# Kernel tuning notes

Measured on AMD Instinct MI355X. Metric: run time of the kernel, lower is better.

## Reference

```python
import jax, jax.numpy as jnp
import numpy as np

B, LQ, LK, H = 8, 2048, 2048, 1024


def setup_inputs() -> dict:
    key = jax.random.key(0)
    kq, kk, kv, km, kw = jax.random.split(key, 5)
    input_Q = jax.random.normal(kq, (B, LQ, H), dtype=jnp.float32)
    input_K = jax.random.normal(kk, (B, LK, H), dtype=jnp.float32)
    input_V = jax.random.normal(kv, (B, LK, H), dtype=jnp.float32)
    mask = jax.random.randint(km, (B, LK), 0, 2, dtype=jnp.int32)
    # learned parameter w_omega [H, H]; scaled init so scores are O(1)-ish
    w_omega = jax.random.normal(kw, (H, H), dtype=jnp.float32) * (H ** -0.5)
    return {"input_Q": input_Q, "input_K": input_K, "input_V": input_V,
            "w_omega": w_omega, "mask": mask}


def reference(input_Q, input_K, input_V, w_omega, mask):
    # att_input = Q @ W : [B, Lq, H]
    att_input = jnp.einsum('bqh,hd->bqd', input_Q, w_omega)
    # scores = att_input @ K^T : [B, Lq, Lk]
    att_scores = jnp.einsum('bqd,bkd->bqk', att_input, input_K)
    # masked fill with -inf where mask == 0 (mask broadcast over query dim)
    neg_inf = jnp.asarray(-jnp.inf, dtype=att_scores.dtype)
    scores = jnp.where(mask[:, None, :] == 0, neg_inf, att_scores)
    probs_softmax = jax.nn.softmax(scores, axis=-1)          # [B, Lq, Lk]
    probs_sigmoid = jax.nn.sigmoid(scores)                   # sigmoid(-inf)=0
    probs_sigmoid_hat = (probs_sigmoid > 0.5).astype(probs_softmax.dtype)
    att_output_softmax = jnp.einsum('bqk,bkh->bqh', probs_softmax, input_V)
    att_output_sigmoid = jnp.einsum('bqk,bkh->bqh', probs_sigmoid_hat, input_V)
    # torch .squeeze(1) is a no-op here since Lq > 1
    return (att_output_softmax, att_output_sigmoid, probs_softmax, probs_sigmoid)
```

## Files before the change

kernel.cpp:

```cpp
#include <hip/hip_runtime.h>
#include <math.h>

#define B_  8
#define LQ_ 2048
#define LK_ 2048
#define H_  1024

#define TAU      4e-3f
#define FIX_CAP  32768
#define FIX_E    8
#define SCL      256.0f
#define SCLQ     16.0f
#define INV_SS   (1.0f / 1048576.0f)

#define KBLK 512

typedef unsigned short ushort_t;
typedef __attribute__((ext_vector_type(8))) _Float16 v8h;
typedef __attribute__((ext_vector_type(8))) short  v8s;
typedef __attribute__((ext_vector_type(4))) float  v4f;
typedef __attribute__((ext_vector_type(4))) float  f4;
typedef __attribute__((ext_vector_type(4))) int    i4;
typedef __attribute__((ext_vector_type(4))) short  s4;

#if defined(__has_builtin)
#if __has_builtin(__builtin_amdgcn_global_load_lds)
#define HAS_GLDS 1
#endif
#endif

__device__ __forceinline__ ushort_t f2bf(float x) {
  unsigned u = __float_as_uint(x);
  u = (u + 0x7FFFu + ((u >> 16) & 1u)) >> 16;
  return (ushort_t)u;
}
__device__ __forceinline__ void split2h(float x, ushort_t& h, ushort_t& l) {
  union { _Float16 f; ushort_t u; } a, b;
  a.f = (_Float16)x;
  b.f = (_Float16)(x - (float)a.f);
  h = a.u; l = b.u;
}

__device__ __forceinline__ void gld_lds16(void* lds_dst, const void* g_src) {
#ifdef HAS_GLDS
  __builtin_amdgcn_global_load_lds((const __attribute__((address_space(1))) void*)g_src,
                                   (__attribute__((address_space(3))) void*)lds_dst,
                                   16, 0, 0);
#else
  *(i4*)lds_dst = *(const i4*)g_src;
#endif
}

__global__ void k_zero(int* p) { *p = 0; }

__global__ void k_split(const float* __restrict__ x, ushort_t* __restrict__ hi,
                        ushort_t* __restrict__ lo, int n4, float scale) {
  int stride = gridDim.x * blockDim.x;
  for (int i = blockIdx.x * blockDim.x + threadIdx.x; i < n4; i += stride) {
    f4 v = ((const f4*)x)[i];
    s4 h, l;
#pragma unroll
    for (int j = 0; j < 4; j++) {
      ushort_t hb, lb; split2h(v[j] * scale, hb, lb);
      h[j] = (short)hb; l[j] = (short)lb;
    }
    ((s4*)hi)[i] = h;
    ((s4*)lo)[i] = l;
  }
}

template <int SPLIT>
__global__ void k_transpose(const float* __restrict__ X, ushort_t* __restrict__ Yhi,
                            ushort_t* __restrict__ Ylo, int R, int C, float scale) {
  __shared__ float t[32][33];
  const int b = blockIdx.z;
  const float* Xb = X + (size_t)b * R * C;
  ushort_t* Yh = Yhi + (size_t)b * R * C;
  const int c0 = blockIdx.x * 32, r0 = blockIdx.y * 32;
  const int tx = threadIdx.x, ty = threadIdx.y;
#pragma unroll
  for (int i = 0; i < 4; i++)
    t[ty + 8 * i][tx] = Xb[(size_t)(r0 + ty + 8 * i) * C + c0 + tx];
  __syncthreads();
#pragma unroll
  for (int i = 0; i < 4; i++) {
    float v = t[tx][ty + 8 * i] * scale;
    size_t o = (size_t)(c0 + ty + 8 * i) * R + r0 + tx;
    if (SPLIT) {
      ushort_t h, l; split2h(v, h, l);
      Yh[o] = h;
      (Ylo + (size_t)b * R * C)[o] = l;
    } else {
      Yh[o] = f2bf(v);
    }
  }
}


template <int EPI>
__global__ __launch_bounds__(256, 2)
void gemm_hx2(const ushort_t* __restrict__ Ahi, const ushort_t* __restrict__ Alo,
              const ushort_t* __restrict__ Bhi, const ushort_t* __restrict__ Blo,
              int KD, long strideAB, long strideBB, int N,
              ushort_t* __restrict__ OutHi, ushort_t* __restrict__ OutLo, long strideOB,
              float* __restrict__ S, float* __restrict__ G, ushort_t* __restrict__ Hatb,
              const int* __restrict__ mask, int* __restrict__ cnt, int* __restrict__ flist) {
  const int b  = blockIdx.z;
  const int m0 = blockIdx.y * 128;
  const int n0 = blockIdx.x * 128;
  const ushort_t* Ah = Ahi + (size_t)b * strideAB + (size_t)m0 * KD;
  const ushort_t* Al = Alo + (size_t)b * strideAB + (size_t)m0 * KD;
  const ushort_t* Bh = Bhi + (size_t)b * strideBB + (size_t)n0 * KD;
  const ushort_t* Bl = Blo + (size_t)b * strideBB + (size_t)n0 * KD;

  __shared__ ushort_t sAh[128 * 32], sAl[128 * 32], sBh[128 * 32], sBl[128 * 32];

  const int tid  = threadIdx.x;
  const int lane = tid & 63;
  const int wid  = tid >> 6;
  const int wm   = (wid >> 1) * 64;
  const int wn   = (wid & 1) * 64;

  v4f acc[4][4] = {};

  const int r1 = tid >> 2;
  const int c1 = (tid & 3) ^ ((tid >> 3) & 3);
  const size_t go1 = (size_t)r1 * KD + (size_t)(c1 * 8);
  const size_t go2 = (size_t)(r1 + 64) * KD + (size_t)(c1 * 8);
  const int ldst1 = tid * 16;
  const int ldst2 = 4096 + tid * 16;

  const int fr = lane & 15;
  const int cq = lane >> 4;

  for (int k0 = 0; k0 < KD; k0 += 32) {
    __syncthreads();
    gld_lds16((char*)sAh + ldst1, Ah + go1 + k0);
    gld_lds16((char*)sAh + ldst2, Ah + go2 + k0);
    gld_lds16((char*)sAl + ldst1, Al + go1 + k0);
    gld_lds16((char*)sAl + ldst2, Al + go2 + k0);
    gld_lds16((char*)sBh + ldst1, Bh + go1 + k0);
    gld_lds16((char*)sBh + ldst2, Bh + go2 + k0);
    gld_lds16((char*)sBl + ldst1, Bl + go1 + k0);
    gld_lds16((char*)sBl + ldst2, Bl + go2 + k0);
    __syncthreads();

    v8h a_h[4], a_l[4], b_h[4], b_l[4];
#pragma unroll
    for (int i = 0; i < 4; i++) {
      const int Ra = wm + i * 16 + fr;
      const int ca = Ra * 32 + (((cq ^ ((Ra >> 1) & 3))) << 3);
      a_h[i] = *(const v8h*)&sAh[ca];
      a_l[i] = *(const v8h*)&sAl[ca];
      const int Rb = wn + i * 16 + fr;
      const int cb = Rb * 32 + (((cq ^ ((Rb >> 1) & 3))) << 3);
      b_h[i] = *(const v8h*)&sBh[cb];
      b_l[i] = *(const v8h*)&sBl[cb];
    }
#pragma unroll
    for (int i = 0; i < 4; i++)
#pragma unroll
      for (int j = 0; j < 4; j++) {
        acc[i][j] = __builtin_amdgcn_mfma_f32_16x16x32_f16(a_h[i], b_h[j], acc[i][j], 0, 0, 0);
        acc[i][j] = __builtin_amdgcn_mfma_f32_16x16x32_f16(a_h[i], b_l[j], acc[i][j], 0, 0, 0);
        acc[i][j] = __builtin_amdgcn_mfma_f32_16x16x32_f16(a_l[i], b_h[j], acc[i][j], 0, 0, 0);
      }
  }

  const int rg = (lane >> 4) * 4;
#pragma unroll
  for (int i = 0; i < 4; i++)
#pragma unroll
    for (int j = 0; j < 4; j++)
#pragma unroll
      for (int r = 0; r < 4; r++) {
        const int grow = m0 + wm + i * 16 + rg + r;
        const int gcol = n0 + wn + j * 16 + fr;
        const float v = acc[i][j][r];
        if (EPI == 0) {
          size_t o = (size_t)b * strideOB + (size_t)grow * N + gcol;
          ushort_t h, l; split2h(v, h, l);
          OutHi[o] = h; OutLo[o] = l;
        } else {
          size_t o = ((size_t)b * LQ_ + grow) * N + gcol;
          const float sv = v * INV_SS;
          S[o] = sv;
          int mk = mask[b * N + gcol];
          const float g = mk ? 1.0f / (1.0f + expf(-sv)) : 0.0f;
          G[o] = g;
          Hatb[o] = (g > 0.5f) ? (ushort_t)0x3F80 : (ushort_t)0;
          if (mk && fabsf(sv) < TAU) {
            int idx = atomicAdd(cnt, 1);
            if (idx < FIX_CAP) flist[idx] = (b << 22) | (grow << 11) | gcol;
          }
        }
      }
}

__global__ __launch_bounds__(256)
void k_fix_blas(const int* __restrict__ cnt, const int* __restrict__ flist,
                const float* __restrict__ Q, const float* __restrict__ Kx,
                const float* __restrict__ W, float* __restrict__ S,
                float* __restrict__ G, ushort_t* __restrict__ Hatb) {
  const int n = min(*cnt, FIX_CAP);
  const int base = blockIdx.x * FIX_E;
  if (base >= n) return;
  const int ne = min(FIX_E, n - base);
  const int tid = threadIdx.x;

  __shared__ float qs[FIX_E][H_];
  __shared__ float aA[FIX_E][H_];
  __shared__ int   ent[FIX_E];

  if (tid < FIX_E) ent[tid] = flist[base + ((tid < ne) ? tid : 0)];
  __syncthreads();

  for (int e = 0; e < FIX_E; e++) {
    const int en = ent[e];
    const int b = en >> 22, q = (en >> 11) & 2047;
    const float* Qr = Q + ((size_t)b * LQ_ + q) * H_;
    for (int i = tid; i < H_; i += 256) qs[e][i] = Qr[i];
  }
  __syncthreads();

  float atot[FIX_E][4];
  float acc[FIX_E][4];
  const float* Wp = W + tid * 4;
#pragma unroll
  for (int blk = 0; blk < 2; blk++) {
    const int h0 = blk * KBLK;
    const int h1 = h0 + KBLK;
#pragma unroll
    for (int e = 0; e < FIX_E; e++)
#pragma unroll
      for (int j = 0; j < 4; j++) acc[e][j] = 0.f;
    for (int h = h0; h < h1; h++) {
      f4 w = *(const f4*)(Wp + (size_t)h * H_);
#pragma unroll
      for (int e = 0; e < FIX_E; e++) {
        const float qv = qs[e][h];
        acc[e][0] = fmaf(qv, w[0], acc[e][0]);
        acc[e][1] = fmaf(qv, w[1], acc[e][1]);
        acc[e][2] = fmaf(qv, w[2], acc[e][2]);
        acc[e][3] = fmaf(qv, w[3], acc[e][3]);
      }
    }
#pragma unroll
    for (int e = 0; e < FIX_E; e++)
#pragma unroll
      for (int j = 0; j < 4; j++)
        atot[e][j] = (blk == 0) ? acc[e][j] : __fadd_rn(atot[e][j], acc[e][j]);
  }
#pragma unroll
  for (int e = 0; e < FIX_E; e++) {
    aA[e][tid * 4 + 0] = atot[e][0];
    aA[e][tid * 4 + 1] = atot[e][1];
    aA[e][tid * 4 + 2] = atot[e][2];
    aA[e][tid * 4 + 3] = atot[e][3];
  }
  __syncthreads();

  if (tid < ne) {
    const int e = tid;
    const int en = ent[e];
    const int b = en >> 22, q = (en >> 11) & 2047, k = en & 2047;
    const float* Kr = Kx + ((size_t)b * LK_ + k) * H_;
    const float* Ar = aA[e];
    float stot = 0.f;
#pragma unroll
    for (int blk = 0; blk < 2; blk++) {
      const int d0 = blk * KBLK;
      const int d1 = d0 + KBLK;
      float a = 0.f;
#pragma unroll 16
      for (int d = d0; d < d1; d++) a = fmaf(Ar[d], Kr[d], a);
      stot = (blk == 0) ? a : __fadd_rn(stot, a);
    }
    size_t o = ((size_t)b * LQ_ + q) * LK_ + k;
    S[o] = stot;
    const float g = 1.0f / (1.0f + expf(-stot));
    G[o] = g;
    Hatb[o] = (g > 0.5f) ? (ushort_t)0x3F80 : (ushort_t)0;
  }
}

__global__ void k_softmax(float* __restrict__ S, const int* __restrict__ mask,
                          ushort_t* __restrict__ Pb) {
  const int row = blockIdx.x;
  const int b   = row >> 11;
  float* Sr = S + (size_t)row * LK_;
  const int* mr = mask + b * LK_;
  const int tid = threadIdx.x;
  const int c0 = tid * 8;

  float v[8]; int mk[8];
  f4 v0 = *(const f4*)&Sr[c0];
  f4 v1 = *(const f4*)&Sr[c0 + 4];
  i4 m0 = *(const i4*)&mr[c0];
  i4 m1 = *(const i4*)&mr[c0 + 4];
#pragma unroll
  for (int j = 0; j < 4; j++) { v[j] = v0[j]; v[4 + j] = v1[j]; mk[j] = m0[j]; mk[4 + j] = m1[j]; }

  float mx = -INFINITY;
#pragma unroll
  for (int j = 0; j < 8; j++) if (mk[j]) mx = fmaxf(mx, v[j]);
#pragma unroll
  for (int off = 32; off; off >>= 1) mx = fmaxf(mx, __shfl_xor(mx, off));
  __shared__ float redm[4], reds[4];
  const int lane = tid & 63, wid = tid >> 6;
  if (lane == 0) redm[wid] = mx;
  __syncthreads();
  mx = fmaxf(fmaxf(redm[0], redm[1]), fmaxf(redm[2], redm[3]));

  float e[8], sum = 0.f;
#pragma unroll
  for (int j = 0; j < 8; j++) { e[j] = mk[j] ? expf(v[j] - mx) : 0.f; sum += e[j]; }
#pragma unroll
  for (int off = 32; off; off >>= 1) sum += __shfl_xor(sum, off);
  if (lane == 0) reds[wid] = sum;
  __syncthreads();
  sum = reds[0] + reds[1] + reds[2] + reds[3];
  const float inv = 1.0f / sum;

  f4 o0, o1;
  v8s pb;
#pragma unroll
  for (int j = 0; j < 4; j++) {
    o0[j] = e[j] * inv; o1[j] = e[4 + j] * inv;
    pb[j] = (short)f2bf(o0[j]); pb[4 + j] = (short)f2bf(o1[j]);
  }
  *(f4*)&Sr[c0] = o0;
  *(f4*)&Sr[c0 + 4] = o1;
  *(v8s*)&Pb[(size_t)row * LK_ + c0] = pb;
}

__global__ __launch_bounds__(256, 2)
void gemm_pvb(const ushort_t* __restrict__ A, const ushort_t* __restrict__ Bt,
              float* __restrict__ O) {
  const int b  = blockIdx.z;
  const int m0 = blockIdx.y * 128;
  const int n0 = blockIdx.x * 128;
  const ushort_t* Ab = A  + ((size_t)b * LQ_ + m0) * (size_t)LK_;
  const ushort_t* Bb = Bt + ((size_t)b * H_  + n0) * (size_t)LK_;

  __shared__ ushort_t sA[128 * 32], sB[128 * 32];

  const int tid  = threadIdx.x;
  const int lane = tid & 63;
  const int wid  = tid >> 6;
  const int wm   = (wid >> 1) * 64;
  const int wn   = (wid & 1) * 64;

  v4f acc[4][4] = {};

  const int r1 = tid >> 2;
  const int c1 = (tid & 3) ^ ((tid >> 3) & 3);
  const size_t go1 = (size_t)r1 * LK_ + (size_t)(c1 * 8);
  const size_t go2 = (size_t)(r1 + 64) * LK_ + (size_t)(c1 * 8);
  const int ldst1 = tid * 16;
  const int ldst2 = 4096 + tid * 16;

  const int fr = lane & 15;
  const int cq = lane >> 4;

  for (int k0 = 0; k0 < LK_; k0 += 32) {
    __syncthreads();
    gld_lds16((char*)sA + ldst1, Ab + go1 + k0);
    gld_lds16((char*)sA + ldst2, Ab + go2 + k0);
    gld_lds16((char*)sB + ldst1, Bb + go1 + k0);
    gld_lds16((char*)sB + ldst2, Bb + go2 + k0);
    __syncthreads();

    v8s af[4], bf[4];
#pragma unroll
    for (int i = 0; i < 4; i++) {
      const int Ra = wm + i * 16 + fr;
      af[i] = *(const v8s*)&sA[Ra * 32 + ((cq ^ ((Ra >> 1) & 3)) << 3)];
      const int Rb = wn + i * 16 + fr;
      bf[i] = *(const v8s*)&sB[Rb * 32 + ((cq ^ ((Rb >> 1) & 3)) << 3)];
    }
#pragma unroll
    for (int i = 0; i < 4; i++)
#pragma unroll
      for (int j = 0; j < 4; j++)
        acc[i][j] = __builtin_amdgcn_mfma_f32_16x16x32_bf16(af[i], bf[j], acc[i][j], 0, 0, 0);
  }

  const int rg = (lane >> 4) * 4;
#pragma unroll
  for (int i = 0; i < 4; i++)
#pragma unroll
    for (int j = 0; j < 4; j++)
#pragma unroll
      for (int r = 0; r < 4; r++) {
        const int grow = m0 + wm + i * 16 + rg + r;
        const int gcol = n0 + wn + j * 16 + fr;
        O[((size_t)b * LQ_ + grow) * H_ + gcol] = acc[i][j][r];
      }
}

extern "C" void kernel_launch(void* const* d_in, const int* in_sizes, int n_in,
                              void* d_out, int out_size, void* d_ws, size_t ws_size,
                              hipStream_t stream) {
  const float* Q = (const float*)d_in[0];
  const float* K = (const float*)d_in[1];
  const float* V = (const float*)d_in[2];
  const float* W = (const float*)d_in[3];
  const int* mask = (const int*)d_in[4];

  float* out0 = (float*)d_out;
  float* out1 = out0 + (size_t)B_ * LQ_ * H_;
  float* out2 = out1 + (size_t)B_ * LQ_ * H_;
  float* out3 = out2 + (size_t)B_ * LQ_ * LK_;

  const size_t NQ = (size_t)B_ * LQ_ * H_;
  char* ws = (char*)d_ws;
  int* cnt   = (int*)ws;                    ws += 256;
  int* flist = (int*)ws;                    ws += FIX_CAP * 4;
  ushort_t* Qhi = (ushort_t*)ws;            ws += NQ * 2;
  ushort_t* Qlo = (ushort_t*)ws;            ws += NQ * 2;
  ushort_t* Khi = (ushort_t*)ws;            ws += NQ * 2;
  ushort_t* Klo = (ushort_t*)ws;            ws += NQ * 2;
  ushort_t* Ahi = (ushort_t*)ws;            ws += NQ * 2;
  ushort_t* Alo = (ushort_t*)ws;            ws += NQ * 2;
  ushort_t* Vt  = (ushort_t*)ws;            ws += NQ * 2;
  ushort_t* Wthi = (ushort_t*)ws;           ws += (size_t)H_ * H_ * 2;
  ushort_t* Wtlo = (ushort_t*)ws;

  ushort_t* hatb = Qhi;
  ushort_t* Pb   = Ahi;

  k_zero<<<1, 1, 0, stream>>>(cnt);

  k_split<<<2048, 256, 0, stream>>>(Q, Qhi, Qlo, (int)(NQ / 4), SCLQ);
  k_split<<<2048, 256, 0, stream>>>(K, Khi, Klo, (int)(NQ / 4), SCL);
  dim3 tb(32, 8);
  k_transpose<1><<<dim3(32, 32, 1), tb, 0, stream>>>(W, Wthi, Wtlo, H_, H_, SCL);
  k_transpose<0><<<dim3(32, 64, B_), tb, 0, stream>>>(V, Vt, nullptr, LK_, H_, 1.0f);

  gemm_hx2<0><<<dim3(H_ / 128, LQ_ / 128, B_), 256, 0, stream>>>(
      Qhi, Qlo, Wthi, Wtlo, H_, (long)LQ_ * H_, 0L, H_,
      Ahi, Alo, (long)LQ_ * H_, nullptr, nullptr, nullptr, nullptr, nullptr, nullptr);

  gemm_hx2<1><<<dim3(LK_ / 128, LQ_ / 128, B_), 256, 0, stream>>>(
      Ahi, Alo, Khi, Klo, H_, (long)LQ_ * H_, (long)LK_ * H_, LK_,
      nullptr, nullptr, 0L, out2, out3, hatb, mask, cnt, flist);

  k_fix_blas<<<FIX_CAP / FIX_E, 256, 0, stream>>>(cnt, flist, Q, K, W, out2, out3, hatb);

  gemm_pvb<<<dim3(H_ / 128, LQ_ / 128, B_), 256, 0, stream>>>(hatb, Vt, out1);

  k_softmax<<<B_ * LQ_, 256, 0, stream>>>(out2, mask, Pb);

  gemm_pvb<<<dim3(H_ / 128, LQ_ / 128, B_), 256, 0, stream>>>(Pb, Vt, out0);
}
```

Baseline: 963.6 us.

## Fuse both PV GEMMs into one kernel and remap blocks across XCDs

The two P@V GEMMs (softmax probs and the sigmoid hat) are merged into a single kernel that loads each V^T tile once and accumulates into two accumulator sets. This saves one full pass over V^T and one launch. A block-index remap is also added to both GEMM kernels so that consecutive tiles land on the same XCD for L2 locality. In exchange, accumulator registers double (32 v4f) and LDS grows by half, which risks spills or lower occupancy under launch_bounds(256,2).

```diff
diff --git a/kernel.cpp b/kernel.cpp
--- a/kernel.cpp
+++ b/kernel.cpp
@@ -49,6 +49,17 @@
 #else
   *(i4*)lds_dst = *(const i4*)g_src;
 #endif
+}
+
+__device__ __forceinline__ void xcd_remap(int& bx, int& by, int& bz) {
+  const int nx = gridDim.x, ny = gridDim.y;
+  const int nwg = nx * ny * gridDim.z;
+  const int hwid = bx + nx * (by + ny * bz);
+  const int work = (hwid & 7) * (nwg >> 3) + (hwid >> 3);
+  bx = work % nx;
+  const int t = work / nx;
+  by = t % ny;
+  bz = t / ny;
 }
 
 __global__ void k_zero(int* p) { *p = 0; }
@@ -105,9 +116,11 @@
               ushort_t* __restrict__ OutHi, ushort_t* __restrict__ OutLo, long strideOB,
               float* __restrict__ S, float* __restrict__ G, ushort_t* __restrict__ Hatb,
               const int* __restrict__ mask, int* __restrict__ cnt, int* __restrict__ flist) {
-  const int b  = blockIdx.z;
-  const int m0 = blockIdx.y * 128;
-  const int n0 = blockIdx.x * 128;
+  int bx = blockIdx.x, by = blockIdx.y, bz = blockIdx.z;
+  xcd_remap(bx, by, bz);
+  const int b  = bz;
+  const int m0 = by * 128;
+  const int n0 = bx * 128;
   const ushort_t* Ah = Ahi + (size_t)b * strideAB + (size_t)m0 * KD;
   const ushort_t* Al = Alo + (size_t)b * strideAB + (size_t)m0 * KD;
   const ushort_t* Bh = Bhi + (size_t)b * strideBB + (size_t)n0 * KD;
@@ -335,15 +348,19 @@
 }
 
 __global__ __launch_bounds__(256, 2)
-void gemm_pvb(const ushort_t* __restrict__ A, const ushort_t* __restrict__ Bt,
-              float* __restrict__ O) {
-  const int b  = blockIdx.z;
-  const int m0 = blockIdx.y * 128;
-  const int n0 = blockIdx.x * 128;
-  const ushort_t* Ab = A  + ((size_t)b * LQ_ + m0) * (size_t)LK_;
+void gemm_pv2(const ushort_t* __restrict__ P, const ushort_t* __restrict__ Hb,
+              const ushort_t* __restrict__ Bt,
+              float* __restrict__ O0, float* __restrict__ O1) {
+  int bx = blockIdx.x, by = blockIdx.y, bz = blockIdx.z;
+  xcd_remap(bx, by, bz);
+  const int b  = bz;
+  const int m0 = by * 128;
+  const int n0 = bx * 128;
+  const ushort_t* Pa = P  + ((size_t)b * LQ_ + m0) * (size_t)LK_;
+  const ushort_t* Ha = Hb + ((size_t)b * LQ_ + m0) * (size_t)LK_;
   const ushort_t* Bb = Bt + ((size_t)b * H_  + n0) * (size_t)LK_;
 
-  __shared__ ushort_t sA[128 * 32], sB[128 * 32];
+  __shared__ ushort_t sP[128 * 32], sH[128 * 32], sB[128 * 32];
 
   const int tid  = threadIdx.x;
   const int lane = tid & 63;
@@ -351,7 +368,7 @@
   const int wm   = (wid >> 1) * 64;
   const int wn   = (wid & 1) * 64;
 
-  v4f acc[4][4] = {};
+  v4f acc0[4][4] = {}, acc1[4][4] = {};
 
   const int r1 = tid >> 2;
   const int c1 = (tid & 3) ^ ((tid >> 3) & 3);
@@ -365,25 +382,31 @@
 
   for (int k0 = 0; k0 < LK_; k0 += 32) {
     __syncthreads();
-    gld_lds16((char*)sA + ldst1, Ab + go1 + k0);
-    gld_lds16((char*)sA + ldst2, Ab + go2 + k0);
+    gld_lds16((char*)sP + ldst1, Pa + go1 + k0);
+    gld_lds16((char*)sP + ldst2, Pa + go2 + k0);
+    gld_lds16((char*)sH + ldst1, Ha + go1 + k0);
+    gld_lds16((char*)sH + ldst2, Ha + go2 + k0);
     gld_lds16((char*)sB + ldst1, Bb + go1 + k0);
     gld_lds16((char*)sB + ldst2, Bb + go2 + k0);
     __syncthreads();
 
-    v8s af[4], bf[4];
+    v8s pf[4], hf[4], bf[4];
 #pragma unroll
     for (int i = 0; i < 4; i++) {
       const int Ra = wm + i * 16 + fr;
-      af[i] = *(const v8s*)&sA[Ra * 32 + ((cq ^ ((Ra >> 1) & 3)) << 3)];
+      const int ca = Ra * 32 + ((cq ^ ((Ra >> 1) & 3)) << 3);
+      pf[i] = *(const v8s*)&sP[ca];
+      hf[i] = *(const v8s*)&sH[ca];
       const int Rb = wn + i * 16 + fr;
       bf[i] = *(const v8s*)&sB[Rb * 32 + ((cq ^ ((Rb >> 1) & 3)) << 3)];
     }
 #pragma unroll
     for (int i = 0; i < 4; i++)
 #pragma unroll
-      for (int j = 0; j < 4; j++)
-        acc[i][j] = __builtin_amdgcn_mfma_f32_16x16x32_bf16(af[i], bf[j], acc[i][j], 0, 0, 0);
+      for (int j = 0; j < 4; j++) {
+        acc0[i][j] = __builtin_amdgcn_mfma_f32_16x16x32_bf16(pf[i], bf[j], acc0[i][j], 0, 0, 0);
+        acc1[i][j] = __builtin_amdgcn_mfma_f32_16x16x32_bf16(hf[i], bf[j], acc1[i][j], 0, 0, 0);
+      }
   }
 
   const int rg = (lane >> 4) * 4;
@@ -395,7 +418,9 @@
       for (int r = 0; r < 4; r++) {
         const int grow = m0 + wm + i * 16 + rg + r;
         const int gcol = n0 + wn + j * 16 + fr;
-        O[((size_t)b * LQ_ + grow) * H_ + gcol] = acc[i][j][r];
+        const size_t o = ((size_t)b * LQ_ + grow) * H_ + gcol;
+        O0[o] = acc0[i][j][r];
+        O1[o] = acc1[i][j][r];
       }
 }
 
@@ -448,9 +473,7 @@
 
   k_fix_blas<<<FIX_CAP / FIX_E, 256, 0, stream>>>(cnt, flist, Q, K, W, out2, out3, hatb);
 
-  gemm_pvb<<<dim3(H_ / 128, LQ_ / 128, B_), 256, 0, stream>>>(hatb, Vt, out1);
-
   k_softmax<<<B_ * LQ_, 256, 0, stream>>>(out2, mask, Pb);
 
-  gemm_pvb<<<dim3(H_ / 128, LQ_ / 128, B_), 256, 0, stream>>>(Pb, Vt, out0);
-}
+  gemm_pv2<<<dim3(H_ / 128, LQ_ / 128, B_), 256, 0, stream>>>(Pb, hatb, Vt, out0, out1);
+}
```

After: 927.5 us. -3.8%, faster.
